# Kernel tuning notes

Measured on AMD Instinct MI355X. Metric: run time of the kernel, lower is better.

## Reference

```python
import jax, jax.numpy as jnp
import numpy as np

B = 64      # num graphs
NPG = 800   # nodes per graph
N = B * NPG
EPG = 6400  # edges per graph (avg degree 8)
APG = 64    # feasible actions per graph
H = 4       # attention heads
C = 64      # hidden channels per head
OUT = 128   # out_channels


def _gat_params(key, fin, h, c, concat):
    k1, k2, k3 = jax.random.split(key, 3)
    s = 1.0 / np.sqrt(fin)
    W = jax.random.uniform(k1, (fin, h * c), jnp.float32, -s, s)
    a_src = jax.random.uniform(k2, (h, c), jnp.float32, -s, s)
    a_dst = jax.random.uniform(k3, (h, c), jnp.float32, -s, s)
    b = jnp.zeros((h * c if concat else c,), jnp.float32)
    return W, a_src, a_dst, b


def _lin_params(key, fin, fout):
    k1, k2 = jax.random.split(key)
    s = 1.0 / np.sqrt(fin)
    W = jax.random.uniform(k1, (fin, fout), jnp.float32, -s, s)
    b = jax.random.uniform(k2, (fout,), jnp.float32, -s, s)
    return W, b


def setup_inputs() -> dict:
    key = jax.random.key(0)
    ks = list(jax.random.split(key, 24))
    x = jax.random.normal(ks[0], (N, 5), jnp.float32)
    offs = jnp.arange(B, dtype=jnp.int32) * NPG
    src = jax.random.randint(ks[1], (B, EPG), 0, NPG, jnp.int32) + offs[:, None]
    dst = jax.random.randint(ks[2], (B, EPG), 0, NPG, jnp.int32) + offs[:, None]
    edge_index = jnp.stack([src.reshape(-1), dst.reshape(-1)])
    batch = jnp.repeat(jnp.arange(B, dtype=jnp.int32), NPG)
    actions_idx = (jax.random.randint(ks[3], (B, APG, 2), 0, NPG, jnp.int32)
                   + offs[:, None, None]).reshape(-1, 2)
    tabu_label = (jax.random.uniform(ks[4], (B * APG, 1)) < 0.5).astype(jnp.float32)
    inp = dict(x=x, edge_index=edge_index, batch=batch,
               actions_idx=actions_idx, tabu_label=tabu_label)
    names = ['f1', 'f2', 'f3', 'b1', 'b2', 'b3']
    fins = [3, H * C, H * C, 3, H * C, H * C]
    hs = [H, H, 1, H, H, 1]
    cs = [C, C, OUT, C, C, OUT]
    concats = [True, True, False, True, True, False]
    for i, nm in enumerate(names):
        W, a_s, a_d, b = _gat_params(ks[5 + i], fins[i], hs[i], cs[i], concats[i])
        inp[nm + '_W'] = W; inp[nm + '_as'] = a_s; inp[nm + '_ad'] = a_d; inp[nm + '_b'] = b
    dims = [(8 * OUT + 1, 2 * OUT), (2 * OUT, 2 * OUT), (2 * OUT, 2 * OUT), (2 * OUT, 1)]
    for i, (fi, fo) in enumerate(dims):
        W, b = _lin_params(ks[12 + i], fi, fo)
        inp['p_W%d' % (i + 1)] = W; inp['p_b%d' % (i + 1)] = b
    return inp


def _gat(h, s, d, W, a_src, a_dst, bias, concat):
    # PyG GATConv: project, per-edge attention, softmax over target index, scatter-add
    n = h.shape[0]
    Hh, Cc = a_src.shape
    xp = (h @ W).reshape(n, Hh, Cc)                      # [N,H,C]
    al_s = (xp * a_src).sum(-1)                          # [N,H]
    al_d = (xp * a_dst).sum(-1)                          # [N,H]
    e = jax.nn.leaky_relu(al_s[s] + al_d[d], 0.2)        # [E,H]
    m = jax.ops.segment_max(e, d, num_segments=n)
    ex = jnp.exp(e - m[d])
    den = jax.ops.segment_sum(ex, d, num_segments=n)
    alpha = ex / (den[d] + 1e-16)
    out = jax.ops.segment_sum(xp[s] * alpha[..., None], d, num_segments=n)  # [N,H,C]
    out = out.reshape(n, Hh * Cc) if concat else out.mean(axis=1)
    return out + bias


def reference(x, edge_index, batch, actions_idx, tabu_label,
              f1_W, f1_as, f1_ad, f1_b, f2_W, f2_as, f2_ad, f2_b,
              f3_W, f3_as, f3_ad, f3_b, b1_W, b1_as, b1_ad, b1_b,
              b2_W, b2_as, b2_ad, b2_b, b3_W, b3_as, b3_ad, b3_b,
              p_W1, p_b1, p_W2, p_b2, p_W3, p_b3, p_W4, p_b4):
    n = x.shape[0]
    ar = jnp.arange(n, dtype=edge_index.dtype)
    ei = jnp.concatenate([edge_index, jnp.stack([ar, ar])], axis=1)  # add_self_loops
    src, dst = ei[0], ei[1]
    # forward branch (flow source_to_target)
    hf = x[:, jnp.array([0, 1, 3])]
    hf = jax.nn.elu(_gat(hf, src, dst, f1_W, f1_as, f1_ad, f1_b, True))
    hf = jax.nn.elu(_gat(hf, src, dst, f2_W, f2_as, f2_ad, f2_b, True))
    hf3 = _gat(hf, src, dst, f3_W, f3_as, f3_ad, f3_b, False)
    # backward branch (flow target_to_source == reversed edges)
    hb = x[:, jnp.array([0, 2, 4])]
    hb = jax.nn.elu(_gat(hb, dst, src, b1_W, b1_as, b1_ad, b1_b, True))
    hb = jax.nn.elu(_gat(hb, dst, src, b2_W, b2_as, b2_ad, b2_b, True))
    hb3 = _gat(hb, dst, src, b3_W, b3_as, b3_ad, b3_b, False)
    h_node = jnp.concatenate([hf3, hb3], axis=-1)        # [N, 2*OUT]
    counts = jax.ops.segment_sum(jnp.ones((n,), x.dtype), batch, num_segments=B)
    g_pool = jax.ops.segment_sum(h_node, batch, num_segments=B) / counts[:, None]
    node_h = jnp.concatenate([h_node, g_pool[batch]], axis=-1)  # [N, 4*OUT]
    action_h = jnp.concatenate([node_h[actions_idx[:, 0]],
                                node_h[actions_idx[:, 1]],
                                tabu_label], axis=-1)    # [A, 8*OUT+1]
    h = jnp.tanh(action_h @ p_W1 + p_b1)
    h = jnp.tanh(h @ p_W2 + p_b2)
    h = jnp.tanh(h @ p_W3 + p_b3)
    score = (h @ p_W4 + p_b4).reshape(B, APG)
    log_prob = jax.nn.log_softmax(score, axis=-1)        # [B, APG]
    entropy = -(jnp.exp(log_prob) * log_prob).sum(-1, keepdims=True)  # [B,1]
    return (log_prob, entropy)
```

## Files before the change

kernel.cpp:

```cpp
#include <hip/hip_runtime.h>
#include <hip/hip_bf16.h>
#include <math.h>

constexpr int NN  = 51200;
constexpr int EE  = 409600;
constexpr int BB  = 64;
constexpr int APG = 64;
constexpr int NPG = 800;
constexpr int SCAN_N = 2 * NN;
constexpr int NA = BB * APG;
constexpr int KF = 1056;

typedef __bf16 bf16x8 __attribute__((ext_vector_type(8)));
typedef float f32x4 __attribute__((ext_vector_type(4)));
typedef float f32x2 __attribute__((ext_vector_type(2)));
typedef __attribute__((address_space(1))) const void g_void;
typedef __attribute__((address_space(3))) void l_void;

__device__ __forceinline__ float leaky(float x) { return fmaxf(x, 0.2f * x); }
__device__ __forceinline__ float bflo(unsigned w) { return __uint_as_float(w << 16); }
__device__ __forceinline__ float bfhi(unsigned w) { return __uint_as_float(w & 0xffff0000u); }
__device__ __forceinline__ unsigned short f2b(float x) {
  __hip_bfloat16 h = __float2bfloat16(x);
  unsigned short u;
  __builtin_memcpy(&u, &h, 2);
  return u;
}
__device__ __forceinline__ unsigned pack2(float a, float b) {
  return (unsigned)f2b(a) | ((unsigned)f2b(b) << 16);
}

__global__ void count_kernel(const int* __restrict__ ei, int* cnt) {
  int e = blockIdx.x * blockDim.x + threadIdx.x;
  if (e >= EE) return;
  int s = ei[e], d = ei[EE + e];
  atomicAdd(&cnt[d], 1);
  atomicAdd(&cnt[NN + s], 1);
}

__global__ __launch_bounds__(256) void scan1_kernel(const int* __restrict__ cnt,
                                                    int* __restrict__ rp,
                                                    int* __restrict__ bsum) {
  __shared__ int wsum[4];
  int b = blockIdx.x, t = threadIdx.x;
  int base = b * 1024 + t * 4;
  int4 v = *(const int4*)(cnt + base);
  int s = v.x + v.y + v.z + v.w;
  int lane = t & 63, wv = t >> 6;
  int incl = s;
  for (int off = 1; off < 64; off <<= 1) {
    int u = __shfl_up(incl, off);
    if (lane >= off) incl += u;
  }
  if (lane == 63) wsum[wv] = incl;
  __syncthreads();
  int woff = 0;
  for (int i = 0; i < wv; i++) woff += wsum[i];
  int excl = woff + incl - s;
  rp[base] = excl;
  rp[base + 1] = excl + v.x;
  rp[base + 2] = excl + v.x + v.y;
  rp[base + 3] = excl + v.x + v.y + v.z;
  if (t == 255) bsum[b] = woff + incl;
}

__global__ void scan2_kernel(const int* __restrict__ bsum, int* __restrict__ boff,
                             int* __restrict__ rp) {
  __shared__ int w0;
  int t = threadIdx.x;
  int v = (t < 100) ? bsum[t] : 0;
  int lane = t & 63;
  int incl = v;
  for (int off = 1; off < 64; off <<= 1) {
    int u = __shfl_up(incl, off);
    if (lane >= off) incl += u;
  }
  if (t == 63) w0 = incl;
  __syncthreads();
  int excl = incl - v + ((t >= 64) ? w0 : 0);
  if (t < 100) boff[t] = excl;
  if (t == 99) rp[SCAN_N] = excl + v;
}

__global__ __launch_bounds__(256) void scan3_kernel(int* __restrict__ rp,
                                                    const int* __restrict__ boff) {
  int b = blockIdx.x;
  int off = boff[b];
  int i = b * 1024 + threadIdx.x * 4;
  int4 v = *(int4*)(rp + i);
  v.x += off; v.y += off; v.z += off; v.w += off;
  *(int4*)(rp + i) = v;
}

__global__ void fill_kernel(const int* __restrict__ ei, const int* __restrict__ rp,
                            int* pos, int* __restrict__ col) {
  int e = blockIdx.x * blockDim.x + threadIdx.x;
  if (e >= EE) return;
  int s = ei[e], d = ei[EE + e];
  int p = atomicAdd(&pos[d], 1);
  col[rp[d] + p] = s;
  int q = atomicAdd(&pos[NN + s], 1);
  col[rp[NN + s] + q] = d;
}

__global__ __launch_bounds__(256) void precomp_kernel(const float* __restrict__ Wf,
                                                      const float* __restrict__ Wb,
                                                      const float* __restrict__ asf,
                                                      const float* __restrict__ adf,
                                                      const float* __restrict__ asb,
                                                      const float* __restrict__ adb,
                                                      float* __restrict__ wa) {
  int wave = (blockIdx.x * blockDim.x + threadIdx.x) >> 6;
  int lane = threadIdx.x & 63;
  if (wave >= 48) return;
  int dir = wave / 24, sd = (wave / 12) % 2, h = (wave / 3) % 4, c = wave % 3;
  const float* W = dir ? Wb : Wf;
  const float* a = dir ? (sd ? adb : asb) : (sd ? adf : asf);
  float v = W[c * 256 + h * 64 + lane] * a[h * 64 + lane];
  for (int off = 1; off < 64; off <<= 1) v += __shfl_xor(v, off);
  if (lane == 0) wa[wave] = v;
}

__global__ __launch_bounds__(256) void lin1_kernel(const float* __restrict__ x,
                                                   const float* __restrict__ Wf,
                                                   const float* __restrict__ Wb,
                                                   const float* __restrict__ wa,
                                                   __hip_bfloat16* __restrict__ out,
                                                   float* __restrict__ al_s,
                                                   float* __restrict__ al_d) {
  int idx = blockIdx.x * 256 + threadIdx.x;
  int n = idx >> 5, grp = idx & 31;
  int dir = (n >= NN) ? 1 : 0;
  int node = dir ? n - NN : n;
  const float* W = dir ? Wb : Wf;
  int c1 = dir ? 2 : 1, c2 = dir ? 4 : 3;
  float f0 = x[node * 5], f1 = x[node * 5 + c1], f2 = x[node * 5 + c2];
  int j0 = grp * 8;
  float v[8];
#pragma unroll
  for (int j = 0; j < 8; j++)
    v[j] = f0 * W[j0 + j] + f1 * W[256 + j0 + j] + f2 * W[512 + j0 + j];
  uint4 u;
  u.x = pack2(v[0], v[1]);
  u.y = pack2(v[2], v[3]);
  u.z = pack2(v[4], v[5]);
  u.w = pack2(v[6], v[7]);
  *(uint4*)(out + (size_t)n * 256 + j0) = u;
  if (grp < 4) {
    const float* ws = wa + dir * 24 + grp * 3;
    const float* wd = wa + dir * 24 + 12 + grp * 3;
    al_s[n * 4 + grp] = f0 * ws[0] + f1 * ws[1] + f2 * ws[2];
    al_d[n * 4 + grp] = f0 * wd[0] + f1 * wd[1] + f2 * wd[2];
  }
}

template <int HH>
__global__ __launch_bounds__(256) void alpha_kernel(const float* __restrict__ als,
                                                    const float* __restrict__ ald,
                                                    const int* __restrict__ rp,
                                                    const int* __restrict__ col,
                                                    float* __restrict__ alpha,
                                                    float* __restrict__ alpha_self) {
  int b = blockIdx.x;
  int xcd = b & 7, q = b >> 3;
  int g2 = (q / 25) * 8 + xcd;
  int d = g2 * 800 + (q % 25) * 32 + (threadIdx.x >> 3);
  int slot = threadIdx.x & 7;
  int off_row = (d >= NN) ? NN : 0;
  float ald_loc[HH], self_w[HH];
#pragma unroll
  for (int h = 0; h < HH; h++) {
    ald_loc[h] = ald[d * HH + h];
    self_w[h] = __expf(leaky(als[d * HH + h] + ald_loc[h]));
  }
  int beg = rp[d], end = rp[d + 1];
  int i0 = beg + slot;
  bool have = i0 < end;
  int s0 = col[have ? i0 : beg] + off_row;
  float sm[HH], w0[HH];
#pragma unroll
  for (int h = 0; h < HH; h++) sm[h] = 0.f;
  if (have) {
#pragma unroll
    for (int h = 0; h < HH; h++) {
      w0[h] = __expf(leaky(als[s0 * HH + h] + ald_loc[h]));
      sm[h] += w0[h];
    }
  }
  for (int i = i0 + 8; i < end; i += 8) {
    int s = col[i] + off_row;
#pragma unroll
    for (int h = 0; h < HH; h++) {
      float w = __expf(leaky(als[s * HH + h] + ald_loc[h]));
      sm[h] += w;
      alpha[(size_t)i * HH + h] = w;
    }
  }
#pragma unroll
  for (int h = 0; h < HH; h++) {
    sm[h] += __shfl_xor(sm[h], 1);
    sm[h] += __shfl_xor(sm[h], 2);
    sm[h] += __shfl_xor(sm[h], 4);
  }
  float inv[HH];
#pragma unroll
  for (int h = 0; h < HH; h++)
    inv[h] = 1.f / (sm[h] + self_w[h] + 1e-16f);
  if (have) {
#pragma unroll
    for (int h = 0; h < HH; h++) alpha[(size_t)i0 * HH + h] = w0[h] * inv[h];
  }
  for (int i = i0 + 8; i < end; i += 8)
#pragma unroll
    for (int h = 0; h < HH; h++) alpha[(size_t)i * HH + h] *= inv[h];
  if (slot == 0) {
#pragma unroll
    for (int h = 0; h < HH; h++)
      alpha_self[d * HH + h] = self_w[h] * inv[h];
  }
}

template <int ND>
__device__ __forceinline__ void load_dw(const unsigned* p, unsigned* w) {
  if constexpr (ND == 4) {
    uint4 v = *(const uint4*)p;
    w[0] = v.x; w[1] = v.y; w[2] = v.z; w[3] = v.w;
  } else {
    uint2 v = *(const uint2*)p;
    w[0] = v.x; w[1] = v.y;
  }
}
__device__ __forceinline__ f32x2 unpk(unsigned w) {
  f32x2 v;
  v.x = bflo(w);
  v.y = bfhi(w);
  return v;
}

template <int HH, int CC, int OUT_SPLIT>
__global__ __launch_bounds__(256) void spmm_kernel(const __hip_bfloat16* __restrict__ xp,
                                                   const float* __restrict__ alpha,
                                                   const float* __restrict__ alpha_self,
                                                   const int* __restrict__ rp,
                                                   const int* __restrict__ col,
                                                   const float* __restrict__ biasf,
                                                   const float* __restrict__ biasb,
                                                   __hip_bfloat16* __restrict__ out_bf,
                                                   int do_elu) {
  constexpr int HC = HH * CC;
  constexpr int CPL = HC / 32;
  constexpr int NW = CPL / 2;
  int b = blockIdx.x;
  int xcd = b & 7, q = b >> 3;
  int g2 = (q / 200) * 8 + xcd;
  int d = g2 * 800 + (q % 200) * 4 + (threadIdx.x >> 6);
  int off_row = (d >= NN) ? NN : 0;
  const float* bias = (d >= NN) ? biasb : biasf;
  int lane = threadIdx.x & 63;
  int sub = lane & 31, g = lane >> 5;
  int h_l = (sub * CPL) / CC;
  const unsigned* xw = (const unsigned*)xp;
  size_t rowoff = (size_t)sub * NW;
  f32x2 acc[NW];
#pragma unroll
  for (int j = 0; j < NW; j++) acc[j] = (f32x2)(0.f);
  int beg = rp[d], end = rp[d + 1];
  int deg = end - beg;
  if (g == 0) {
    float a = alpha_self[d * HH + h_l];
    unsigned w[NW];
    load_dw<NW>(xw + (size_t)d * (HC / 2) + rowoff, w);
#pragma unroll
    for (int q2 = 0; q2 < NW; q2++) acc[q2] += a * unpk(w[q2]);
  }
  for (int it = 0; it * 4 < deg; it++) {
    int e1 = beg + it * 4 + g;
    int e2 = e1 + 2;
    bool p1 = e1 < end, p2 = e2 < end;
    int ec1 = p1 ? e1 : beg, ec2 = p2 ? e2 : beg;
    int s1 = col[ec1] + off_row, s2 = col[ec2] + off_row;
    float a1 = p1 ? alpha[(size_t)ec1 * HH + h_l] : 0.f;
    float a2 = p2 ? alpha[(size_t)ec2 * HH + h_l] : 0.f;
    unsigned w1[NW], w2[NW];
    load_dw<NW>(xw + (size_t)s1 * (HC / 2) + rowoff, w1);
    load_dw<NW>(xw + (size_t)s2 * (HC / 2) + rowoff, w2);
#pragma unroll
    for (int q2 = 0; q2 < NW; q2++)
      acc[q2] += a1 * unpk(w1[q2]) + a2 * unpk(w2[q2]);
  }
#pragma unroll
  for (int j = 0; j < NW; j++) {
    acc[j].x += __shfl_xor(acc[j].x, 32);
    acc[j].y += __shfl_xor(acc[j].y, 32);
  }
  if (g == 0) {
    float v[CPL];
#pragma unroll
    for (int j = 0; j < NW; j++) {
      v[2 * j] = acc[j].x + bias[sub * CPL + 2 * j];
      v[2 * j + 1] = acc[j].y + bias[sub * CPL + 2 * j + 1];
    }
    if (do_elu) {
#pragma unroll
      for (int j = 0; j < CPL; j++) v[j] = v[j] > 0.f ? v[j] : (__expf(v[j]) - 1.f);
    }
    unsigned* ob;
    if constexpr (OUT_SPLIT) {
      int nd = (d < NN) ? d : d - NN;
      int oo = (d < NN) ? 0 : 64;
      ob = (unsigned*)out_bf + (size_t)nd * 128 + oo + sub * NW;
    } else {
      ob = (unsigned*)out_bf + (size_t)d * (HC / 2) + rowoff;
    }
#pragma unroll
    for (int q2 = 0; q2 < NW; q2++)
      ob[q2] = pack2(v[2 * q2], v[2 * q2 + 1]);
  }
}

__global__ void castW2_kernel(const float* __restrict__ W0, const float* __restrict__ W1,
                              __hip_bfloat16* __restrict__ Wt0,
                              __hip_bfloat16* __restrict__ Wt1,
                              int K, int N, int Kp) {
  int idx = blockIdx.x * 256 + threadIdx.x;
  int tot = N * Kp;
  if (idx >= 2 * tot) return;
  const float* W = (idx < tot) ? W0 : W1;
  __hip_bfloat16* Wt = (idx < tot) ? Wt0 : Wt1;
  int i = (idx < tot) ? idx : idx - tot;
  int n = i / Kp, k = i % Kp;
  Wt[i] = (k < K) ? __float2bfloat16(W[(size_t)k * N + n]) : __float2bfloat16(0.f);
}

__global__ void castW1_kernel(const float* __restrict__ W, __hip_bfloat16* __restrict__ Wt,
                              int K, int N, int Kp) {
  int idx = blockIdx.x * 256 + threadIdx.x;
  if (idx >= N * Kp) return;
  int n = idx / Kp, k = idx % Kp;
  Wt[idx] = (k < K) ? __float2bfloat16(W[(size_t)k * N + n]) : __float2bfloat16(0.f);
}

template <int EPI, int ALH, int ALCC>
__global__ __launch_bounds__(256) void gemm_mfma(const __hip_bfloat16* __restrict__ A,
                                                 const __hip_bfloat16* __restrict__ Bt0,
                                                 const __hip_bfloat16* __restrict__ Bt1,
                                                 __hip_bfloat16* __restrict__ Cb,
                                                 const float* __restrict__ bias0,
                                                 const float* __restrict__ bias1,
                                                 const float* __restrict__ asv0,
                                                 const float* __restrict__ asv1,
                                                 const float* __restrict__ adv0,
                                                 const float* __restrict__ adv1,
                                                 float* __restrict__ al_s,
                                                 float* __restrict__ al_d,
                                                 int M, int N, int K, int Mhalf) {
  __shared__ __align__(16) __hip_bfloat16 As[128 * 32];
  __shared__ __align__(16) __hip_bfloat16 Bs[128 * 32];
  int t = threadIdx.x;
  int wave = t >> 6, lane = t & 63;
  int wm = (wave >> 1) * 64, wn = (wave & 1) * 64;
  int bm = blockIdx.y * 128, bn = blockIdx.x * 128;
  bool second = bm >= Mhalf;
  const __hip_bfloat16* Bt = second ? Bt1 : Bt0;
  const float* bias = second ? bias1 : bias0;
  const float* asv = second ? asv1 : asv0;
  const float* adv = second ? adv1 : adv0;

  int r0 = t >> 2, c0 = (t & 3) * 8;
  const __hip_bfloat16* Ag0 = A + (size_t)(bm + r0) * K + c0;
  const __hip_bfloat16* Ag1 = A + (size_t)(bm + r0 + 64) * K + c0;
  const __hip_bfloat16* Bg0 = Bt + (size_t)(bn + r0) * K + c0;
  const __hip_bfloat16* Bg1 = Bt + (size_t)(bn + r0 + 64) * K + c0;
  __hip_bfloat16* Asp0 = As + t * 8;
  __hip_bfloat16* Asp1 = As + 64 * 8 * 4 + t * 8;
  __hip_bfloat16* Bsp0 = Bs + t * 8;
  __hip_bfloat16* Bsp1 = Bs + 64 * 8 * 4 + t * 8;

  f32x4 acc[4][4];
#pragma unroll
  for (int i = 0; i < 4; i++)
#pragma unroll
    for (int j = 0; j < 4; j++) acc[i][j] = (f32x4)(0.f);

  int frag_off = (lane & 15) * 32 + (lane >> 4) * 8;
  const __hip_bfloat16* Ab = As + wm * 32 + frag_off;
  const __hip_bfloat16* Bb = Bs + wn * 32 + frag_off;

  for (int k0 = 0; k0 < K; k0 += 32) {
    __syncthreads();
    __builtin_amdgcn_global_load_lds((g_void*)(Ag0 + k0), (l_void*)Asp0, 16, 0, 0);
    __builtin_amdgcn_global_load_lds((g_void*)(Ag1 + k0), (l_void*)Asp1, 16, 0, 0);
    __builtin_amdgcn_global_load_lds((g_void*)(Bg0 + k0), (l_void*)Bsp0, 16, 0, 0);
    __builtin_amdgcn_global_load_lds((g_void*)(Bg1 + k0), (l_void*)Bsp1, 16, 0, 0);
    __syncthreads();
    bf16x8 af[4], bfr[4];
#pragma unroll
    for (int i = 0; i < 4; i++) af[i] = *(const bf16x8*)(Ab + i * 16 * 32);
#pragma unroll
    for (int j = 0; j < 4; j++) bfr[j] = *(const bf16x8*)(Bb + j * 16 * 32);
#pragma unroll
    for (int i = 0; i < 4; i++)
#pragma unroll
      for (int j = 0; j < 4; j++)
        acc[i][j] = __builtin_amdgcn_mfma_f32_16x16x32_bf16(af[i], bfr[j], acc[i][j], 0, 0, 0);
  }

  int cr = (lane >> 4) * 4, cc = lane & 15;

  if constexpr (ALH > 0) {
    int head = (bn + wn) / ALCC;
    float as_c[4], ad_c[4];
#pragma unroll
    for (int j = 0; j < 4; j++) {
      int colx = bn + wn + j * 16 + cc;
      as_c[j] = asv[colx];
      ad_c[j] = adv[colx];
    }
#pragma unroll
    for (int i = 0; i < 4; i++)
#pragma unroll
      for (int r = 0; r < 4; r++) {
        float ps = 0.f, pd = 0.f;
#pragma unroll
        for (int j = 0; j < 4; j++) {
          ps += acc[i][j][r] * as_c[j];
          pd += acc[i][j][r] * ad_c[j];
        }
        ps += __shfl_xor(ps, 1); pd += __shfl_xor(pd, 1);
        ps += __shfl_xor(ps, 2); pd += __shfl_xor(pd, 2);
        ps += __shfl_xor(ps, 4); pd += __shfl_xor(pd, 4);
        ps += __shfl_xor(ps, 8); pd += __shfl_xor(pd, 8);
        if ((lane & 15) == 0) {
          int row = bm + wm + i * 16 + cr + r;
          if (ALCC > 64) {
            atomicAdd(&al_s[row * ALH + head], ps);
            atomicAdd(&al_d[row * ALH + head], pd);
          } else {
            al_s[row * ALH + head] = ps;
            al_d[row * ALH + head] = pd;
          }
        }
      }
  }

#pragma unroll
  for (int i = 0; i < 4; i++)
#pragma unroll
    for (int j = 0; j < 4; j++) {
      int colx = bn + wn + j * 16 + cc;
      float bs = (EPI == 2) ? bias[colx] : 0.f;
#pragma unroll
      for (int r = 0; r < 4; r++) {
        float v = acc[i][j][r];
        if (EPI == 2) v = tanhf(v + bs);
        Cb[(size_t)(bm + wm + i * 16 + cr + r) * N + colx] = __float2bfloat16(v);
      }
    }
}

__global__ void pool1_kernel(const __hip_bfloat16* __restrict__ h_node,
                             float* __restrict__ part) {
  int g = blockIdx.y, c = blockIdx.x, t = threadIdx.x;
  const unsigned* base = (const unsigned*)h_node + ((size_t)g * NPG + c * 100) * 128 + t;
  f32x2 s = (f32x2)(0.f);
  for (int i = 0; i < 100; i++) s += unpk(base[(size_t)i * 128]);
  part[(size_t)(g * 8 + c) * 256 + 2 * t] = s.x;
  part[(size_t)(g * 8 + c) * 256 + 2 * t + 1] = s.y;
}

__global__ void pool2_kernel(const float* __restrict__ part, float* __restrict__ g_pool) {
  int g = blockIdx.x, t = threadIdx.x;
  float s = 0.f;
  for (int c = 0; c < 8; c++) s += part[(size_t)(g * 8 + c) * 256 + t];
  g_pool[g * 256 + t] = s * (1.f / NPG);
}

__global__ __launch_bounds__(256) void buildfeat_kernel(const __hip_bfloat16* __restrict__ h_node,
                                                        const float* __restrict__ g_pool,
                                                        const int* __restrict__ actions,
                                                        const float* __restrict__ tabu,
                                                        const int* __restrict__ batch,
                                                        __hip_bfloat16* __restrict__ feat) {
  int a = (blockIdx.x * blockDim.x + threadIdx.x) >> 6;
  int lane = threadIdx.x & 63;
  if (a >= NA) return;
  int n0 = actions[a * 2], n1 = actions[a * 2 + 1];
  int g = batch[n0];
  ushort4 v0 = *(const ushort4*)(h_node + (size_t)n0 * 256 + lane * 4);
  float4 vg = *(const float4*)(g_pool + (size_t)g * 256 + lane * 4);
  ushort4 v1 = *(const ushort4*)(h_node + (size_t)n1 * 256 + lane * 4);
  __hip_bfloat16* fr = feat + (size_t)a * KF;
  ushort4 ug = make_ushort4(f2b(vg.x), f2b(vg.y), f2b(vg.z), f2b(vg.w));
  *(ushort4*)(fr + lane * 4) = v0;
  *(ushort4*)(fr + 256 + lane * 4) = ug;
  *(ushort4*)(fr + 512 + lane * 4) = v1;
  *(ushort4*)(fr + 768 + lane * 4) = ug;
  if (lane < 8) {
    float t0 = (lane == 0) ? tabu[a] : 0.f;
    ushort4 u = make_ushort4(f2b(t0), 0, 0, 0);
    *(ushort4*)(fr + 1024 + lane * 4) = u;
  }
}

__global__ __launch_bounds__(256) void head_kernel(const __hip_bfloat16* __restrict__ y,
                                                   const float* __restrict__ W4,
                                                   const float* __restrict__ b4,
                                                   float* __restrict__ out) {
  __shared__ float sc[64];
  int g = blockIdx.x;
  int t = threadIdx.x;
  int a = t >> 2, sub = t & 3;
  int aid = g * 64 + a;
  const unsigned* row = (const unsigned*)(y + (size_t)aid * 256) + sub * 32;
  const float* w = W4 + sub * 64;
  float s = 0.f;
#pragma unroll
  for (int q = 0; q < 32; q++) {
    s += bflo(row[q]) * w[2 * q] + bfhi(row[q]) * w[2 * q + 1];
  }
  s += __shfl_xor(s, 1);
  s += __shfl_xor(s, 2);
  if (sub == 0) sc[a] = s + b4[0];
  __syncthreads();
  if (t < 64) {
    float v = sc[t];
    float m = v;
    for (int off = 1; off < 64; off <<= 1) m = fmaxf(m, __shfl_xor(m, off));
    float ex = expf(v - m);
    float sum = ex;
    for (int off = 1; off < 64; off <<= 1) sum += __shfl_xor(sum, off);
    float lp = v - m - logf(sum);
    out[g * 64 + t] = lp;
    float pe = (ex / sum) * lp;
    for (int off = 1; off < 64; off <<= 1) pe += __shfl_xor(pe, off);
    if (t == 0) out[BB * APG + g] = -pe;
  }
}

extern "C" void kernel_launch(void* const* d_in, const int* in_sizes, int n_in,
                              void* d_out, int out_size, void* d_ws, size_t ws_size,
                              hipStream_t stream) {
  const float* x = (const float*)d_in[0];
  const int* ei = (const int*)d_in[1];
  const int* batch = (const int*)d_in[2];
  const int* actions = (const int*)d_in[3];
  const float* tabu = (const float*)d_in[4];
  const float* fW[3] = {(const float*)d_in[5], (const float*)d_in[9], (const float*)d_in[13]};
  const float* fas[3] = {(const float*)d_in[6], (const float*)d_in[10], (const float*)d_in[14]};
  const float* fad[3] = {(const float*)d_in[7], (const float*)d_in[11], (const float*)d_in[15]};
  const float* fb[3] = {(const float*)d_in[8], (const float*)d_in[12], (const float*)d_in[16]};
  const float* bW[3] = {(const float*)d_in[17], (const float*)d_in[21], (const float*)d_in[25]};
  const float* bas[3] = {(const float*)d_in[18], (const float*)d_in[22], (const float*)d_in[26]};
  const float* bad[3] = {(const float*)d_in[19], (const float*)d_in[23], (const float*)d_in[27]};
  const float* bb[3] = {(const float*)d_in[20], (const float*)d_in[24], (const float*)d_in[28]};
  const float* pW1 = (const float*)d_in[29];
  const float* pb1 = (const float*)d_in[30];
  const float* pW2 = (const float*)d_in[31];
  const float* pb2 = (const float*)d_in[32];
  const float* pW3 = (const float*)d_in[33];
  const float* pb3 = (const float*)d_in[34];
  const float* pW4 = (const float*)d_in[35];
  const float* pb4 = (const float*)d_in[36];
  float* out = (float*)d_out;

  char* ws = (char*)d_ws;
  size_t o = 0;
  auto alloc = [&](size_t bytes) -> void* {
    o = (o + 255) & ~(size_t)255;
    void* p = ws + o;
    o += bytes;
    return p;
  };
  int* cnt = (int*)alloc((size_t)4 * NN * 4);
  int* rp = (int*)alloc((size_t)(SCAN_N + 1) * 4);
  int* col = (int*)alloc(((size_t)2 * EE + 64) * 4);
  int* bsum = (int*)alloc(128 * 4);
  int* boff = (int*)alloc(128 * 4);
  float* al_s = (float*)alloc((size_t)SCAN_N * 4 * 4);
  float* al_d = (float*)alloc((size_t)SCAN_N * 4 * 4);
  float* alpha = (float*)alloc((size_t)2 * EE * 4 * 4);
  float* alpha_self = (float*)alloc((size_t)SCAN_N * 4 * 4);
  float* wa = (float*)alloc(64 * 4);
  __hip_bfloat16* xp = (__hip_bfloat16*)alloc((size_t)SCAN_N * 256 * 2);
  __hip_bfloat16* bufA = (__hip_bfloat16*)alloc((size_t)SCAN_N * 256 * 2);
  __hip_bfloat16* h_node = (__hip_bfloat16*)alloc((size_t)NN * 256 * 2);
  __hip_bfloat16* wt0 = (__hip_bfloat16*)alloc((size_t)256 * KF * 2);
  __hip_bfloat16* wt1 = (__hip_bfloat16*)alloc((size_t)256 * KF * 2);
  float* part = (float*)alloc((size_t)BB * 8 * 256 * 4);
  float* g_pool = (float*)alloc((size_t)BB * 256 * 4);
  __hip_bfloat16* feat = xp;
  __hip_bfloat16* y1 = feat + (size_t)NA * KF;
  __hip_bfloat16* y2 = y1 + (size_t)NA * 256;

  hipMemsetAsync(cnt, 0, (size_t)4 * NN * 4, stream);
  count_kernel<<<(EE + 255) / 256, 256, 0, stream>>>(ei, cnt);
  scan1_kernel<<<SCAN_N / 1024, 256, 0, stream>>>(cnt, rp, bsum);
  scan2_kernel<<<1, 128, 0, stream>>>(bsum, boff, rp);
  scan3_kernel<<<SCAN_N / 1024, 256, 0, stream>>>(rp, boff);
  fill_kernel<<<(EE + 255) / 256, 256, 0, stream>>>(ei, rp, cnt + 2 * NN, col);

  const int nwb = SCAN_N / 4;
  const int nab = SCAN_N * 8 / 256;

  precomp_kernel<<<12, 256, 0, stream>>>(fW[0], bW[0], fas[0], fad[0], bas[0], bad[0], wa);
  lin1_kernel<<<SCAN_N * 32 / 256, 256, 0, stream>>>(x, fW[0], bW[0], wa, xp, al_s, al_d);
  alpha_kernel<4><<<nab, 256, 0, stream>>>(al_s, al_d, rp, col, alpha, alpha_self);
  spmm_kernel<4, 64, 0><<<nwb, 256, 0, stream>>>(xp, alpha, alpha_self, rp, col,
                                                 fb[0], bb[0], bufA, 1);
  castW2_kernel<<<(2 * 256 * 256 + 255) / 256, 256, 0, stream>>>(fW[1], bW[1], wt0, wt1,
                                                                 256, 256, 256);
  gemm_mfma<1, 4, 64><<<dim3(2, SCAN_N / 128), 256, 0, stream>>>(
      bufA, wt0, wt1, xp, nullptr, nullptr, fas[1], bas[1], fad[1], bad[1],
      al_s, al_d, SCAN_N, 256, 256, NN);
  alpha_kernel<4><<<nab, 256, 0, stream>>>(al_s, al_d, rp, col, alpha, alpha_self);
  spmm_kernel<4, 64, 0><<<nwb, 256, 0, stream>>>(xp, alpha, alpha_self, rp, col,
                                                 fb[1], bb[1], bufA, 1);
  castW2_kernel<<<(2 * 128 * 256 + 255) / 256, 256, 0, stream>>>(fW[2], bW[2], wt0, wt1,
                                                                 256, 128, 256);
  hipMemsetAsync(al_s, 0, (size_t)2 * SCAN_N * 4, stream);
  gemm_mfma<1, 1, 128><<<dim3(1, SCAN_N / 128), 256, 0, stream>>>(
      bufA, wt0, wt1, xp, nullptr, nullptr, fas[2], bas[2], fad[2], bad[2],
      al_s, al_d, SCAN_N, 128, 256, NN);
  alpha_kernel<1><<<nab, 256, 0, stream>>>(al_s, al_d, rp, col, alpha, alpha_self);
  spmm_kernel<1, 128, 1><<<nwb, 256, 0, stream>>>(xp, alpha, alpha_self, rp, col,
                                                  fb[2], bb[2], h_node, 0);

  pool1_kernel<<<dim3(8, BB), 128, 0, stream>>>(h_node, part);
  pool2_kernel<<<BB, 256, 0, stream>>>(part, g_pool);

  buildfeat_kernel<<<NA / 4, 256, 0, stream>>>(h_node, g_pool, actions, tabu, batch, feat);
  castW1_kernel<<<(256 * KF + 255) / 256, 256, 0, stream>>>(pW1, wt0, 1025, 256, KF);
  gemm_mfma<2, 0, 64><<<dim3(2, NA / 128), 256, 0, stream>>>(
      feat, wt0, wt0, y1, pb1, pb1, nullptr, nullptr, nullptr, nullptr,
      nullptr, nullptr, NA, 256, KF, 1 << 30);
  castW2_kernel<<<(2 * 256 * 256 + 255) / 256, 256, 0, stream>>>(pW2, pW3, wt0, wt1,
                                                                 256, 256, 256);
  gemm_mfma<2, 0, 64><<<dim3(2, NA / 128), 256, 0, stream>>>(
      y1, wt0, wt0, y2, pb2, pb2, nullptr, nullptr, nullptr, nullptr,
      nullptr, nullptr, NA, 256, 256, 1 << 30);
  gemm_mfma<2, 0, 64><<<dim3(2, NA / 128), 256, 0, stream>>>(
      y2, wt1, wt1, y1, pb3, pb3, nullptr, nullptr, nullptr, nullptr,
      nullptr, nullptr, NA, 256, 256, 1 << 30);
  head_kernel<<<BB, 256, 0, stream>>>(y1, pW4, pb4, out);
}
```

Measured before the change: 530.4 us.

## Restructure SpMM to full-wavefront rows with shuffle-broadcast indices and batched gathers

The SpMM kernel now gives each destination row to a full 64-lane wavefront that covers all channels, instead of two half-waves splitting edges and merging with a cross-half shuffle. Column indices and attention weights are loaded once cooperatively, then broadcast with lane shuffles. Up to 16 row gathers are issued before any are consumed, to raise memory-level parallelism. Edges beyond 64 fall back to a serial loop. The cost is more registers for the 16 in-flight loads and divergent predication for small degrees.

Result: no change. 520.3 us (-1.9%).

```diff
diff --git a/kernel.cpp b/kernel.cpp
--- a/kernel.cpp
+++ b/kernel.cpp
@@ -220,16 +220,6 @@
   }
 }
 
-template <int ND>
-__device__ __forceinline__ void load_dw(const unsigned* p, unsigned* w) {
-  if constexpr (ND == 4) {
-    uint4 v = *(const uint4*)p;
-    w[0] = v.x; w[1] = v.y; w[2] = v.z; w[3] = v.w;
-  } else {
-    uint2 v = *(const uint2*)p;
-    w[0] = v.x; w[1] = v.y;
-  }
-}
 __device__ __forceinline__ f32x2 unpk(unsigned w) {
   f32x2 v;
   v.x = bflo(w);
@@ -248,8 +238,8 @@
                                                    __hip_bfloat16* __restrict__ out_bf,
                                                    int do_elu) {
   constexpr int HC = HH * CC;
-  constexpr int CPL = HC / 32;
-  constexpr int NW = CPL / 2;
+  constexpr int DWL = HC / 128;
+  constexpr int RDW = HC / 2;
   int b = blockIdx.x;
   int xcd = b & 7, q = b >> 3;
   int g2 = (q / 200) * 8 + xcd;
@@ -257,64 +247,113 @@
   int off_row = (d >= NN) ? NN : 0;
   const float* bias = (d >= NN) ? biasb : biasf;
   int lane = threadIdx.x & 63;
-  int sub = lane & 31, g = lane >> 5;
-  int h_l = (sub * CPL) / CC;
+  int hsel = (HH == 4) ? (lane >> 4) : 0;
   const unsigned* xw = (const unsigned*)xp;
-  size_t rowoff = (size_t)sub * NW;
-  f32x2 acc[NW];
-#pragma unroll
-  for (int j = 0; j < NW; j++) acc[j] = (f32x2)(0.f);
-  int beg = rp[d], end = rp[d + 1];
+
+  int beg = __builtin_amdgcn_readfirstlane(rp[d]);
+  int end = __builtin_amdgcn_readfirstlane(rp[d + 1]);
   int deg = end - beg;
-  if (g == 0) {
-    float a = alpha_self[d * HH + h_l];
-    unsigned w[NW];
-    load_dw<NW>(xw + (size_t)d * (HC / 2) + rowoff, w);
-#pragma unroll
-    for (int q2 = 0; q2 < NW; q2++) acc[q2] += a * unpk(w[q2]);
-  }
-  for (int it = 0; it * 4 < deg; it++) {
-    int e1 = beg + it * 4 + g;
-    int e2 = e1 + 2;
-    bool p1 = e1 < end, p2 = e2 < end;
-    int ec1 = p1 ? e1 : beg, ec2 = p2 ? e2 : beg;
-    int s1 = col[ec1] + off_row, s2 = col[ec2] + off_row;
-    float a1 = p1 ? alpha[(size_t)ec1 * HH + h_l] : 0.f;
-    float a2 = p2 ? alpha[(size_t)ec2 * HH + h_l] : 0.f;
-    unsigned w1[NW], w2[NW];
-    load_dw<NW>(xw + (size_t)s1 * (HC / 2) + rowoff, w1);
-    load_dw<NW>(xw + (size_t)s2 * (HC / 2) + rowoff, w2);
-#pragma unroll
-    for (int q2 = 0; q2 < NW; q2++)
-      acc[q2] += a1 * unpk(w1[q2]) + a2 * unpk(w2[q2]);
-  }
-#pragma unroll
-  for (int j = 0; j < NW; j++) {
-    acc[j].x += __shfl_xor(acc[j].x, 32);
-    acc[j].y += __shfl_xor(acc[j].y, 32);
-  }
-  if (g == 0) {
-    float v[CPL];
-#pragma unroll
-    for (int j = 0; j < NW; j++) {
-      v[2 * j] = acc[j].x + bias[sub * CPL + 2 * j];
-      v[2 * j + 1] = acc[j].y + bias[sub * CPL + 2 * j + 1];
+  int nfast = deg < 64 ? deg : 64;
+
+  float aself = alpha_self[d * HH + hsel];
+  const unsigned* selfp = xw + (size_t)d * RDW + lane * DWL;
+  uint2 sw;
+  if constexpr (DWL == 2) sw = *(const uint2*)selfp;
+  else sw.x = *selfp;
+  int chb = lane * (2 * DWL);
+  float4 bv;
+  if constexpr (DWL == 2) bv = *(const float4*)(bias + chb);
+  else {
+    float2 t = *(const float2*)(bias + chb);
+    bv.x = t.x; bv.y = t.y; bv.z = 0.f; bv.w = 0.f;
+  }
+  int cl = (lane < nfast) ? lane : (nfast > 0 ? nfast - 1 : 0);
+  int colv = col[beg + cl] + off_row;
+  float av = 0.f;
+  if constexpr (HH == 4) {
+    int e15 = lane & 15;
+    if (e15 < nfast) av = alpha[(size_t)(beg + e15) * 4 + hsel];
+  } else {
+    if (lane < nfast) av = alpha[beg + lane];
+  }
+
+  f32x2 acc0 = aself * unpk(sw.x);
+  f32x2 acc1 = (f32x2)(0.f);
+  if constexpr (DWL == 2) acc1 = aself * unpk(sw.y);
+
+#define SPMM_ISS(k)                                          \
+  {                                                          \
+    int jj = c0 + k;                                         \
+    jj = (jj < nfast) ? jj : nfast - 1;                      \
+    int s = __shfl(colv, jj);                                \
+    const unsigned* p = xw + (size_t)s * RDW + lane * DWL;   \
+    if constexpr (DWL == 2) w##k = *(const uint2*)p;         \
+    else w##k.x = *p;                                        \
+  }
+#define SPMM_CNS(k)                                          \
+  {                                                          \
+    float a;                                                 \
+    if constexpr (HH == 4) a = __shfl(av, (lane & 48) | k);  \
+    else a = __shfl(av, c0 + k);                             \
+    acc0 += a * unpk(w##k.x);                                \
+    if constexpr (DWL == 2) acc1 += a * unpk(w##k.y);        \
+  }
+
+  for (int c0 = 0; c0 < nfast; c0 += 16) {
+    int ne = nfast - c0;
+    ne = (ne > 16) ? 16 : ne;
+    if constexpr (HH == 4) {
+      if (c0) {
+        int e15 = lane & 15;
+        av = (c0 + e15 < nfast) ? alpha[(size_t)(beg + c0 + e15) * 4 + hsel] : 0.f;
+      }
     }
-    if (do_elu) {
-#pragma unroll
-      for (int j = 0; j < CPL; j++) v[j] = v[j] > 0.f ? v[j] : (__expf(v[j]) - 1.f);
+    uint2 w0, w1, w2, w3, w4, w5, w6, w7, w8, w9, w10, w11, w12, w13, w14, w15;
+    SPMM_ISS(0) SPMM_ISS(1) SPMM_ISS(2) SPMM_ISS(3)
+    if (ne > 4) { SPMM_ISS(4) SPMM_ISS(5) SPMM_ISS(6) SPMM_ISS(7) }
+    if (ne > 8) { SPMM_ISS(8) SPMM_ISS(9) SPMM_ISS(10) SPMM_ISS(11) }
+    if (ne > 12) { SPMM_ISS(12) SPMM_ISS(13) SPMM_ISS(14) SPMM_ISS(15) }
+    SPMM_CNS(0) SPMM_CNS(1) SPMM_CNS(2) SPMM_CNS(3)
+    if (ne > 4) { SPMM_CNS(4) SPMM_CNS(5) SPMM_CNS(6) SPMM_CNS(7) }
+    if (ne > 8) { SPMM_CNS(8) SPMM_CNS(9) SPMM_CNS(10) SPMM_CNS(11) }
+    if (ne > 12) { SPMM_CNS(12) SPMM_CNS(13) SPMM_CNS(14) SPMM_CNS(15) }
+  }
+#undef SPMM_ISS
+#undef SPMM_CNS
+
+  for (int e = 64; e < deg; e++) {
+    int s = col[beg + e] + off_row;
+    float a = (HH == 4) ? alpha[(size_t)(beg + e) * 4 + hsel] : alpha[beg + e];
+    const unsigned* p = xw + (size_t)s * RDW + lane * DWL;
+    acc0 += a * unpk(p[0]);
+    if constexpr (DWL == 2) acc1 += a * unpk(p[1]);
+  }
+
+  float v0 = acc0.x + bv.x, v1 = acc0.y + bv.y;
+  float v2 = 0.f, v3 = 0.f;
+  if constexpr (DWL == 2) { v2 = acc1.x + bv.z; v3 = acc1.y + bv.w; }
+  if (do_elu) {
+    v0 = v0 > 0.f ? v0 : (__expf(v0) - 1.f);
+    v1 = v1 > 0.f ? v1 : (__expf(v1) - 1.f);
+    if constexpr (DWL == 2) {
+      v2 = v2 > 0.f ? v2 : (__expf(v2) - 1.f);
+      v3 = v3 > 0.f ? v3 : (__expf(v3) - 1.f);
     }
-    unsigned* ob;
-    if constexpr (OUT_SPLIT) {
-      int nd = (d < NN) ? d : d - NN;
-      int oo = (d < NN) ? 0 : 64;
-      ob = (unsigned*)out_bf + (size_t)nd * 128 + oo + sub * NW;
+  }
+  if constexpr (OUT_SPLIT) {
+    int nd = (d < NN) ? d : d - NN;
+    int oo = (d < NN) ? 0 : 64;
+    *((unsigned*)out_bf + (size_t)nd * 128 + oo + lane) = pack2(v0, v1);
+  } else {
+    unsigned* ob = (unsigned*)out_bf + (size_t)d * RDW + lane * DWL;
+    if constexpr (DWL == 2) {
+      uint2 u;
+      u.x = pack2(v0, v1);
+      u.y = pack2(v2, v3);
+      *(uint2*)ob = u;
     } else {
-      ob = (unsigned*)out_bf + (size_t)d * (HC / 2) + rowoff;
+      *ob = pack2(v0, v1);
     }
-#pragma unroll
-    for (int q2 = 0; q2 < NW; q2++)
-      ob[q2] = pack2(v[2 * q2], v[2 * q2 + 1]);
   }
 }
 
```

## Restructure GAT SpMM to half-wave per node with batched neighbor gathers

Applied to the files above, without the earlier changes.

The SpMM kernel now assigns each 32-lane half-wave to one destination node and processes 8 nodes per wave across a loop over 64 nodes per block. Neighbor indices and alpha values are loaded cooperatively and broadcast with shuffles, so 8 row gathers are in flight per iteration. This replaces the old split of each node's edges across two half-waves plus a final cross-half reduction. The lin1 and alpha kernels also loop over several former blocks per block to cut launch and grid overhead. Risks include divergence when the two nodes in a wave have different degrees, extra shuffle cost, and a clamp on column indices.

Result: no change. 534.9 us (+0.9%).

```diff
diff --git a/kernel.cpp b/kernel.cpp
--- a/kernel.cpp
+++ b/kernel.cpp
@@ -128,29 +128,32 @@
                                                    __hip_bfloat16* __restrict__ out,
                                                    float* __restrict__ al_s,
                                                    float* __restrict__ al_d) {
-  int idx = blockIdx.x * 256 + threadIdx.x;
-  int n = idx >> 5, grp = idx & 31;
-  int dir = (n >= NN) ? 1 : 0;
-  int node = dir ? n - NN : n;
-  const float* W = dir ? Wb : Wf;
-  int c1 = dir ? 2 : 1, c2 = dir ? 4 : 3;
-  float f0 = x[node * 5], f1 = x[node * 5 + c1], f2 = x[node * 5 + c2];
-  int j0 = grp * 8;
-  float v[8];
-#pragma unroll
-  for (int j = 0; j < 8; j++)
-    v[j] = f0 * W[j0 + j] + f1 * W[256 + j0 + j] + f2 * W[512 + j0 + j];
-  uint4 u;
-  u.x = pack2(v[0], v[1]);
-  u.y = pack2(v[2], v[3]);
-  u.z = pack2(v[4], v[5]);
-  u.w = pack2(v[6], v[7]);
-  *(uint4*)(out + (size_t)n * 256 + j0) = u;
-  if (grp < 4) {
-    const float* ws = wa + dir * 24 + grp * 3;
-    const float* wd = wa + dir * 24 + 12 + grp * 3;
-    al_s[n * 4 + grp] = f0 * ws[0] + f1 * ws[1] + f2 * ws[2];
-    al_d[n * 4 + grp] = f0 * wd[0] + f1 * wd[1] + f2 * wd[2];
+#pragma unroll 1
+  for (int it = 0; it < 8; ++it) {
+    int idx = blockIdx.x * 2048 + it * 256 + threadIdx.x;
+    int n = idx >> 5, grp = idx & 31;
+    int dir = (n >= NN) ? 1 : 0;
+    int node = dir ? n - NN : n;
+    const float* W = dir ? Wb : Wf;
+    int c1 = dir ? 2 : 1, c2 = dir ? 4 : 3;
+    float f0 = x[node * 5], f1 = x[node * 5 + c1], f2 = x[node * 5 + c2];
+    int j0 = grp * 8;
+    float v[8];
+#pragma unroll
+    for (int j = 0; j < 8; j++)
+      v[j] = f0 * W[j0 + j] + f1 * W[256 + j0 + j] + f2 * W[512 + j0 + j];
+    uint4 u;
+    u.x = pack2(v[0], v[1]);
+    u.y = pack2(v[2], v[3]);
+    u.z = pack2(v[4], v[5]);
+    u.w = pack2(v[6], v[7]);
+    *(uint4*)(out + (size_t)n * 256 + j0) = u;
+    if (grp < 4) {
+      const float* ws = wa + dir * 24 + grp * 3;
+      const float* wd = wa + dir * 24 + 12 + grp * 3;
+      al_s[n * 4 + grp] = f0 * ws[0] + f1 * ws[1] + f2 * ws[2];
+      al_d[n * 4 + grp] = f0 * wd[0] + f1 * wd[1] + f2 * wd[2];
+    }
   }
 }
 
@@ -161,75 +164,68 @@
                                                     const int* __restrict__ col,
                                                     float* __restrict__ alpha,
                                                     float* __restrict__ alpha_self) {
-  int b = blockIdx.x;
-  int xcd = b & 7, q = b >> 3;
-  int g2 = (q / 25) * 8 + xcd;
-  int d = g2 * 800 + (q % 25) * 32 + (threadIdx.x >> 3);
-  int slot = threadIdx.x & 7;
-  int off_row = (d >= NN) ? NN : 0;
-  float ald_loc[HH], self_w[HH];
-#pragma unroll
-  for (int h = 0; h < HH; h++) {
-    ald_loc[h] = ald[d * HH + h];
-    self_w[h] = __expf(leaky(als[d * HH + h] + ald_loc[h]));
-  }
-  int beg = rp[d], end = rp[d + 1];
-  int i0 = beg + slot;
-  bool have = i0 < end;
-  int s0 = col[have ? i0 : beg] + off_row;
-  float sm[HH], w0[HH];
-#pragma unroll
-  for (int h = 0; h < HH; h++) sm[h] = 0.f;
-  if (have) {
+#pragma unroll 1
+  for (int sub_b = 0; sub_b < 4; ++sub_b) {
+    int b = blockIdx.x * 4 + sub_b;
+    int xcd = b & 7, q = b >> 3;
+    int g2 = (q / 25) * 8 + xcd;
+    int d = g2 * 800 + (q % 25) * 32 + (threadIdx.x >> 3);
+    int slot = threadIdx.x & 7;
+    int off_row = (d >= NN) ? NN : 0;
+    float ald_loc[HH], self_w[HH];
 #pragma unroll
     for (int h = 0; h < HH; h++) {
-      w0[h] = __expf(leaky(als[s0 * HH + h] + ald_loc[h]));
-      sm[h] += w0[h];
-    }
-  }
-  for (int i = i0 + 8; i < end; i += 8) {
-    int s = col[i] + off_row;
+      ald_loc[h] = ald[d * HH + h];
+      self_w[h] = __expf(leaky(als[d * HH + h] + ald_loc[h]));
+    }
+    int beg = rp[d], end = rp[d + 1];
+    int i0 = beg + slot;
+    bool have = i0 < end;
+    int s0 = col[have ? i0 : beg] + off_row;
+    float sm[HH], w0[HH];
+#pragma unroll
+    for (int h = 0; h < HH; h++) sm[h] = 0.f;
+    if (have) {
+#pragma unroll
+      for (int h = 0; h < HH; h++) {
+        w0[h] = __expf(leaky(als[s0 * HH + h] + ald_loc[h]));
+        sm[h] += w0[h];
+      }
+    }
+    for (int i = i0 + 8; i < end; i += 8) {
+      int s = col[i] + off_row;
+#pragma unroll
+      for (int h = 0; h < HH; h++) {
+        float w = __expf(leaky(als[s * HH + h] + ald_loc[h]));
+        sm[h] += w;
+        alpha[(size_t)i * HH + h] = w;
+      }
+    }
 #pragma unroll
     for (int h = 0; h < HH; h++) {
-      float w = __expf(leaky(als[s * HH + h] + ald_loc[h]));
-      sm[h] += w;
-      alpha[(size_t)i * HH + h] = w;
-    }
-  }
-#pragma unroll
-  for (int h = 0; h < HH; h++) {
-    sm[h] += __shfl_xor(sm[h], 1);
-    sm[h] += __shfl_xor(sm[h], 2);
-    sm[h] += __shfl_xor(sm[h], 4);
-  }
-  float inv[HH];
-#pragma unroll
-  for (int h = 0; h < HH; h++)
-    inv[h] = 1.f / (sm[h] + self_w[h] + 1e-16f);
-  if (have) {
-#pragma unroll
-    for (int h = 0; h < HH; h++) alpha[(size_t)i0 * HH + h] = w0[h] * inv[h];
-  }
-  for (int i = i0 + 8; i < end; i += 8)
-#pragma unroll
-    for (int h = 0; h < HH; h++) alpha[(size_t)i * HH + h] *= inv[h];
-  if (slot == 0) {
+      sm[h] += __shfl_xor(sm[h], 1);
+      sm[h] += __shfl_xor(sm[h], 2);
+      sm[h] += __shfl_xor(sm[h], 4);
+    }
+    float inv[HH];
 #pragma unroll
     for (int h = 0; h < HH; h++)
-      alpha_self[d * HH + h] = self_w[h] * inv[h];
-  }
-}
-
-template <int ND>
-__device__ __forceinline__ void load_dw(const unsigned* p, unsigned* w) {
-  if constexpr (ND == 4) {
-    uint4 v = *(const uint4*)p;
-    w[0] = v.x; w[1] = v.y; w[2] = v.z; w[3] = v.w;
-  } else {
-    uint2 v = *(const uint2*)p;
-    w[0] = v.x; w[1] = v.y;
-  }
-}
+      inv[h] = 1.f / (sm[h] + self_w[h] + 1e-16f);
+    if (have) {
+#pragma unroll
+      for (int h = 0; h < HH; h++) alpha[(size_t)i0 * HH + h] = w0[h] * inv[h];
+    }
+    for (int i = i0 + 8; i < end; i += 8)
+#pragma unroll
+      for (int h = 0; h < HH; h++) alpha[(size_t)i * HH + h] *= inv[h];
+    if (slot == 0) {
+#pragma unroll
+      for (int h = 0; h < HH; h++)
+        alpha_self[d * HH + h] = self_w[h] * inv[h];
+    }
+  }
+}
+
 __device__ __forceinline__ f32x2 unpk(unsigned w) {
   f32x2 v;
   v.x = bflo(w);
@@ -248,73 +244,110 @@
                                                    __hip_bfloat16* __restrict__ out_bf,
                                                    int do_elu) {
   constexpr int HC = HH * CC;
-  constexpr int CPL = HC / 32;
-  constexpr int NW = CPL / 2;
+  constexpr int RDW = HC / 2;
+  constexpr int DL = RDW / 32;
   int b = blockIdx.x;
-  int xcd = b & 7, q = b >> 3;
-  int g2 = (q / 200) * 8 + xcd;
-  int d = g2 * 800 + (q % 200) * 4 + (threadIdx.x >> 6);
-  int off_row = (d >= NN) ? NN : 0;
-  const float* bias = (d >= NN) ? biasb : biasf;
-  int lane = threadIdx.x & 63;
-  int sub = lane & 31, g = lane >> 5;
-  int h_l = (sub * CPL) / CC;
+  int d0 = ((b & 7) * 200 + (b >> 3)) << 6;
+  int t = threadIdx.x;
+  int wv = t >> 6, lane = t & 63;
+  int sub = lane & 31, halfsel = lane >> 5;
+  int lbase = lane & 32;
+  int off_row = (d0 >= NN) ? NN : 0;
+  const float* bias = (d0 >= NN) ? biasb : biasf;
+  int hsel = (HH == 4) ? (sub >> 3) : 0;
   const unsigned* xw = (const unsigned*)xp;
-  size_t rowoff = (size_t)sub * NW;
-  f32x2 acc[NW];
-#pragma unroll
-  for (int j = 0; j < NW; j++) acc[j] = (f32x2)(0.f);
-  int beg = rp[d], end = rp[d + 1];
-  int deg = end - beg;
-  if (g == 0) {
-    float a = alpha_self[d * HH + h_l];
-    unsigned w[NW];
-    load_dw<NW>(xw + (size_t)d * (HC / 2) + rowoff, w);
-#pragma unroll
-    for (int q2 = 0; q2 < NW; q2++) acc[q2] += a * unpk(w[q2]);
-  }
-  for (int it = 0; it * 4 < deg; it++) {
-    int e1 = beg + it * 4 + g;
-    int e2 = e1 + 2;
-    bool p1 = e1 < end, p2 = e2 < end;
-    int ec1 = p1 ? e1 : beg, ec2 = p2 ? e2 : beg;
-    int s1 = col[ec1] + off_row, s2 = col[ec2] + off_row;
-    float a1 = p1 ? alpha[(size_t)ec1 * HH + h_l] : 0.f;
-    float a2 = p2 ? alpha[(size_t)ec2 * HH + h_l] : 0.f;
-    unsigned w1[NW], w2[NW];
-    load_dw<NW>(xw + (size_t)s1 * (HC / 2) + rowoff, w1);
-    load_dw<NW>(xw + (size_t)s2 * (HC / 2) + rowoff, w2);
-#pragma unroll
-    for (int q2 = 0; q2 < NW; q2++)
-      acc[q2] += a1 * unpk(w1[q2]) + a2 * unpk(w2[q2]);
-  }
-#pragma unroll
-  for (int j = 0; j < NW; j++) {
-    acc[j].x += __shfl_xor(acc[j].x, 32);
-    acc[j].y += __shfl_xor(acc[j].y, 32);
-  }
-  if (g == 0) {
-    float v[CPL];
-#pragma unroll
-    for (int j = 0; j < NW; j++) {
-      v[2 * j] = acc[j].x + bias[sub * CPL + 2 * j];
-      v[2 * j + 1] = acc[j].y + bias[sub * CPL + 2 * j + 1];
+  float bv[2 * DL];
+#pragma unroll
+  for (int j = 0; j < 2 * DL; j++) bv[j] = bias[sub * 2 * DL + j];
+
+#pragma unroll 1
+  for (int it = 0; it < 8; ++it) {
+    int d = d0 + (it * 4 + wv) * 2 + halfsel;
+    int beg = rp[d];
+    int deg = rp[d + 1] - beg;
+    int degmax = max(deg, __shfl_xor(deg, 32));
+    degmax = __builtin_amdgcn_readfirstlane(degmax);
+    float aself = alpha_self[d * HH + hsel];
+    f32x2 acc[DL];
+    {
+      const unsigned* sp = xw + (size_t)d * RDW + sub * DL;
+      if constexpr (DL == 4) {
+        uint4 sw = *(const uint4*)sp;
+        acc[0] = aself * unpk(sw.x);
+        acc[1] = aself * unpk(sw.y);
+        acc[2] = aself * unpk(sw.z);
+        acc[3] = aself * unpk(sw.w);
+      } else {
+        uint2 sw = *(const uint2*)sp;
+        acc[0] = aself * unpk(sw.x);
+        acc[1] = aself * unpk(sw.y);
+      }
+    }
+    for (int c0 = 0; c0 < degmax; c0 += 8) {
+      int ce = c0 + sub;
+      ce = (ce < deg) ? ce : (deg > 0 ? deg - 1 : 0);
+      int colv = col[beg + ce];
+      colv = ((unsigned)colv < (unsigned)NN) ? colv : 0;
+      colv += off_row;
+      float av = 0.f;
+      if constexpr (HH == 4) {
+        int e = c0 + (sub >> 2);
+        if (e < deg) av = alpha[(size_t)(beg + e) * 4 + (sub & 3)];
+      } else {
+        int e = c0 + sub;
+        if (e < deg) av = alpha[beg + e];
+      }
+      uint4 w[8];
+#pragma unroll
+      for (int k = 0; k < 8; k++) {
+        int s = __shfl(colv, lbase + k);
+        const unsigned* p = xw + (size_t)s * RDW + sub * DL;
+        if constexpr (DL == 4) {
+          w[k] = *(const uint4*)p;
+        } else {
+          uint2 v2 = *(const uint2*)p;
+          w[k].x = v2.x;
+          w[k].y = v2.y;
+        }
+      }
+#pragma unroll
+      for (int k = 0; k < 8; k++) {
+        float a;
+        if constexpr (HH == 4) a = __shfl(av, lbase + k * 4 + hsel);
+        else a = __shfl(av, lbase + k);
+        acc[0] += a * unpk(w[k].x);
+        acc[1] += a * unpk(w[k].y);
+        if constexpr (DL == 4) {
+          acc[2] += a * unpk(w[k].z);
+          acc[3] += a * unpk(w[k].w);
+        }
+      }
+    }
+    float v[2 * DL];
+#pragma unroll
+    for (int j = 0; j < DL; j++) {
+      v[2 * j] = acc[j].x + bv[2 * j];
+      v[2 * j + 1] = acc[j].y + bv[2 * j + 1];
     }
     if (do_elu) {
 #pragma unroll
-      for (int j = 0; j < CPL; j++) v[j] = v[j] > 0.f ? v[j] : (__expf(v[j]) - 1.f);
-    }
-    unsigned* ob;
+      for (int j = 0; j < 2 * DL; j++) v[j] = v[j] > 0.f ? v[j] : (__expf(v[j]) - 1.f);
+    }
     if constexpr (OUT_SPLIT) {
       int nd = (d < NN) ? d : d - NN;
       int oo = (d < NN) ? 0 : 64;
-      ob = (unsigned*)out_bf + (size_t)nd * 128 + oo + sub * NW;
+      uint2 u;
+      u.x = pack2(v[0], v[1]);
+      u.y = pack2(v[2], v[3]);
+      *(uint2*)((unsigned*)out_bf + (size_t)nd * 128 + oo + sub * 2) = u;
     } else {
-      ob = (unsigned*)out_bf + (size_t)d * (HC / 2) + rowoff;
-    }
-#pragma unroll
-    for (int q2 = 0; q2 < NW; q2++)
-      ob[q2] = pack2(v[2 * q2], v[2 * q2 + 1]);
+      uint4 u;
+      u.x = pack2(v[0], v[1]);
+      u.y = pack2(v[2], v[3]);
+      u.z = pack2(v[4], v[5]);
+      u.w = pack2(v[6], v[7]);
+      *(uint4*)((unsigned*)out_bf + (size_t)d * RDW + sub * DL) = u;
+    }
   }
 }
 
@@ -599,11 +632,11 @@
   scan3_kernel<<<SCAN_N / 1024, 256, 0, stream>>>(rp, boff);
   fill_kernel<<<(EE + 255) / 256, 256, 0, stream>>>(ei, rp, cnt + 2 * NN, col);
 
-  const int nwb = SCAN_N / 4;
-  const int nab = SCAN_N * 8 / 256;
+  const int nwb = 1600;
+  const int nab = 800;
 
   precomp_kernel<<<12, 256, 0, stream>>>(fW[0], bW[0], fas[0], fad[0], bas[0], bad[0], wa);
-  lin1_kernel<<<SCAN_N * 32 / 256, 256, 0, stream>>>(x, fW[0], bW[0], wa, xp, al_s, al_d);
+  lin1_kernel<<<1600, 256, 0, stream>>>(x, fW[0], bW[0], wa, xp, al_s, al_d);
   alpha_kernel<4><<<nab, 256, 0, stream>>>(al_s, al_d, rp, col, alpha, alpha_self);
   spmm_kernel<4, 64, 0><<<nwb, 256, 0, stream>>>(xp, alpha, alpha_self, rp, col,
                                                  fb[0], bb[0], bufA, 1);
```
